# Performance work log

Hardware: AMD Instinct MI355X
Metric: run time of the kernel (lower is better)

## Reference

```python
import jax, jax.numpy as jnp
import numpy as np

B, N, H, D = 16, 128, 32, 5            # graphs, entities, heads, multi_hop_max_dist
NUM_EDGES, NUM_SPATIAL, NUM_EDGE_DIS = 1536, 512, 128
HID, NEF = 768, 3                       # hidden dim (unused in math), edge feats


def setup_inputs() -> dict:
    key = jax.random.key(0)
    ks = jax.random.split(key, 8)
    x = jax.random.normal(ks[0], (B, N, HID), jnp.float32)
    attn_bias = jax.random.normal(ks[1], (B, N + 1, N + 1), jnp.float32)
    spatial_pos = jax.random.randint(ks[2], (B, N, N), 0, NUM_SPATIAL)
    edge_input = jax.random.randint(ks[3], (B, N, N, D, NEF), 0, NUM_EDGES + 1)
    # embedding tables (std=0.02 init; padding_idx=0 rows zeroed)
    edge_encoder_w = (0.02 * jax.random.normal(ks[4], (NUM_EDGES + 1, H), jnp.float32)).at[0].set(0.0)
    structural_w = (0.02 * jax.random.normal(ks[5], (NUM_SPATIAL, H), jnp.float32)).at[0].set(0.0)
    edge_dis_w = 0.02 * jax.random.normal(ks[6], (NUM_EDGE_DIS * H * H, 1), jnp.float32)
    virt_w = 0.02 * jax.random.normal(ks[7], (1, H), jnp.float32)
    return {"x": x, "attn_bias": attn_bias, "spatial_pos": spatial_pos,
            "edge_input": edge_input, "edge_encoder_w": edge_encoder_w,
            "structural_w": structural_w, "edge_dis_w": edge_dis_w, "virt_w": virt_w}


def reference(x, attn_bias, spatial_pos, edge_input, edge_encoder_w, structural_w, edge_dis_w, virt_w):
    n_graph, n_entity = x.shape[:2]
    # [B, H, N+1, N+1]
    bias = jnp.broadcast_to(attn_bias[:, None], (n_graph, H, n_entity + 1, n_entity + 1))
    # structural (spatial) encoding on the NxN sub-block
    sp_bias = structural_w[spatial_pos].transpose(0, 3, 1, 2)          # [B,H,N,N]
    bias = bias.at[:, :, 1:, 1:].add(sp_bias)
    # graph-token virtual distance
    t = virt_w.reshape(1, H, 1)
    bias = bias.at[:, :, 1:, 0].add(t)
    bias = bias.at[:, :, 0, :].add(t)
    # ---- multi_hop relational encoding ----
    sp = jnp.where(spatial_pos == 0, 1, spatial_pos)
    sp = jnp.where(sp > 1, sp - 1, sp)
    sp = jnp.clip(sp, 0, D)                                            # [B,N,N]
    ei = edge_input[:, :, :, :D, :]                                    # [B,N,N,D,F]
    ei = edge_encoder_w[ei].mean(-2)                                   # [B,N,N,D,H]
    # per-hop head-mixing: bmm over hop dim
    Wdis = edge_dis_w.reshape(-1, H, H)[:D]                            # [D,H,H]
    ei = jnp.einsum('bijdh,dhk->bijdk', ei, Wdis)                      # [B,N,N,D,H]
    ei = ei.sum(-2) / sp[..., None].astype(ei.dtype)                   # [B,N,N,H]
    ei = ei.transpose(0, 3, 1, 2)                                      # [B,H,N,N]
    bias = bias.at[:, :, 1:, 1:].add(ei)
    # final residual add of raw attn_bias
    bias = bias + attn_bias[:, None]
    return bias
```

## Files before the change

kernel.cpp:

```cpp
#include <hip/hip_runtime.h>
#include <hip/hip_bf16.h>

#define B_   16
#define N_   128
#define H_   32
#define D_   5
#define NE1  1537
#define NP1  129

#define QSCALE   2.857142857e-3f
#define QINV     350.0f

#define FQ_BYTES   (D_ * NE1 * 16)
#define FQ_DWORDS  (FQ_BYTES / 4)
#define ST_DWORDS  (512 * 32 * 2 / 4)
#define TOT_DWORDS (FQ_DWORDS + ST_DWORDS)
#define TOT_QUADS  (TOT_DWORDS / 4)

static __device__ __forceinline__ float bits2f(unsigned int u) {
    union { unsigned int ui; float f; } cv; cv.ui = u; return cv.f;
}

struct __attribute__((packed, aligned(4))) pk4 { int x, y, z, w; };
struct __attribute__((packed, aligned(4))) pk2 { int x, y; };

__global__ __launch_bounds__(256) void fused_tab_kernel(
    const float* __restrict__ edge_encoder_w,
    const float* __restrict__ edge_dis_w,
    const float* __restrict__ structural_w,
    unsigned char* __restrict__ fused_q,
    unsigned short* __restrict__ st_bf16)
{
    __shared__ float wd[32 * 32];
    const int tid = threadIdx.x;
    const int bx  = blockIdx.x;

    if (bx >= 965) {
        const int e = (bx - 965) * 256 + tid;
        if (e < 512 * 32) {
            st_bf16[e] = (unsigned short)(
                __hip_bfloat16_raw(__float2bfloat16(structural_w[e])).x);
        }
        return;
    }

    const int d     = bx / 193;
    const int chunk = bx % 193;

    const float* wsrc = edge_dis_w + d * 1024;
    for (int k = tid; k < 1024; k += 256) wd[k] = wsrc[k];
    __syncthreads();

    const int g    = tid >> 5;
    const int lane = tid & 31;
    const int idx  = chunk * 8 + g;
    if (idx >= NE1) return;

    float w = edge_encoder_w[idx * 32 + lane];
    float acc = 0.f;
    #pragma unroll
    for (int hh = 0; hh < 32; ++hh) {
        acc += __shfl(w, hh, 32) * wd[hh * 32 + lane];
    }

    int q = (int)__builtin_rintf(acc * QINV);
    q = (q > 7) ? 7 : ((q < -7) ? -7 : q);
    q += 8;

    const int v0 = __shfl(q, 2 * lane,     32);
    const int v1 = __shfl(q, 2 * lane + 1, 32);
    if (lane < 16) {
        fused_q[(d * NE1 + idx) * 16 + lane] = (unsigned char)(v0 | (v1 << 4));
    }
}

__global__ __launch_bounds__(1024) void main_kernel(
    const float* __restrict__ attn_bias,
    const int*   __restrict__ spatial_pos,
    const int*   __restrict__ edge_input,
    const uint4* __restrict__ wsrc,
    float* __restrict__ out)
{
    __shared__ __align__(16) unsigned int lds[TOT_DWORDS];

    const int tid = threadIdx.x;
    const int bx  = blockIdx.x;

    uint4* ldsq = (uint4*)lds;
    for (int k = tid; k < TOT_QUADS; k += 1024) ldsq[k] = wsrc[k];
    __syncthreads();

    const int cell = bx * 1024 + tid;
    const int b = cell >> 14;
    const int i = (cell >> 7) & 127;
    const int j = cell & 127;

    const int* eip = edge_input + cell * 15;
    const pk4 e03  = *(const pk4*)(eip);
    const pk4 e47  = *(const pk4*)(eip + 4);
    const pk4 e8b  = *(const pk4*)(eip + 8);
    const pk2 ecd  = *(const pk2*)(eip + 12);
    const int ee   = eip[14];
    const int eidx[15] = { e03.x, e03.y, e03.z, e03.w,
                           e47.x, e47.y, e47.z, e47.w,
                           e8b.x, e8b.y, e8b.z, e8b.w,
                           ecd.x, ecd.y, ee };

    const int sp0  = spatial_pos[cell];
    const float ab2 = 2.0f * attn_bias[(b * NP1 + (i + 1)) * NP1 + (j + 1)];

    unsigned int aL0 = 0, aL1 = 0, aL2 = 0, aL3 = 0;
    unsigned int aH0 = 0, aH1 = 0, aH2 = 0, aH3 = 0;
    #pragma unroll
    for (int t = 0; t < 15; ++t) {
        const int d  = t / 3;
        const int ro = (d * NE1 + eidx[t]) * 4;
        const uint4 r = *(const uint4*)&lds[ro];
        aL0 += r.x & 0x0F0F0F0Fu;  aH0 += (r.x >> 4) & 0x0F0F0F0Fu;
        aL1 += r.y & 0x0F0F0F0Fu;  aH1 += (r.y >> 4) & 0x0F0F0F0Fu;
        aL2 += r.z & 0x0F0F0F0Fu;  aH2 += (r.z >> 4) & 0x0F0F0F0Fu;
        aL3 += r.w & 0x0F0F0F0Fu;  aH3 += (r.w >> 4) & 0x0F0F0F0Fu;
    }

    int s = sp0; if (s == 0) s = 1; if (s > 1) s -= 1; if (s > D_) s = D_;
    const float kq = QSCALE * __builtin_amdgcn_rcpf(3.0f * (float)s);
    const float C  = ab2 - 120.0f * kq;

    const uint4* stq = (const uint4*)&lds[FQ_DWORDS];
    const uint4 SQ[4] = { stq[sp0 * 4 + 0], stq[sp0 * 4 + 1],
                          stq[sp0 * 4 + 2], stq[sp0 * 4 + 3] };

    const int obase = (b * 32) * (NP1 * NP1) + (i + 1) * NP1 + (j + 1);
    const unsigned int AL[4] = {aL0, aL1, aL2, aL3};
    const unsigned int AH[4] = {aH0, aH1, aH2, aH3};

    #pragma unroll
    for (int q = 0; q < 4; ++q) {
        const unsigned int sdw[4] = {SQ[q].x, SQ[q].y, SQ[q].z, SQ[q].w};
        #pragma unroll
        for (int bb = 0; bb < 4; ++bb) {
            const int hE = 8 * q + 2 * bb;
            const float stE = bits2f(sdw[bb] << 16) + C;
            const float stO = bits2f(sdw[bb] & 0xFFFF0000u) + C;
            const float vE = (float)((AL[q] >> (8 * bb)) & 255u);
            const float vO = (float)((AH[q] >> (8 * bb)) & 255u);
            out[obase + hE * (NP1 * NP1)]       = vE * kq + stE;
            out[obase + (hE + 1) * (NP1 * NP1)] = vO * kq + stO;
        }
    }
}

__global__ __launch_bounds__(256) void border_kernel(
    const float* __restrict__ attn_bias,
    const float* __restrict__ virt_w,
    float* __restrict__ out)
{
    const int bh = blockIdx.x;
    const int b = bh >> 5;
    const int h = bh & 31;
    const float t = virt_w[h];

    float*       ob = out + (b * H_ + h) * NP1 * NP1;
    const float* ab = attn_bias + b * NP1 * NP1;

    for (int idx = threadIdx.x; idx < NP1 + N_; idx += 256) {
        if (idx < NP1) {
            ob[idx] = 2.0f * ab[idx] + t;
        } else {
            const int i = idx - 128;
            ob[i * NP1] = 2.0f * ab[i * NP1] + t;
        }
    }
}

extern "C" void kernel_launch(void* const* d_in, const int* in_sizes, int n_in,
                              void* d_out, int out_size, void* d_ws, size_t ws_size,
                              hipStream_t stream) {
    const float* attn_bias      = (const float*)d_in[1];
    const int*   spatial_pos    = (const int*)  d_in[2];
    const int*   edge_input     = (const int*)  d_in[3];
    const float* edge_encoder_w = (const float*)d_in[4];
    const float* structural_w   = (const float*)d_in[5];
    const float* edge_dis_w     = (const float*)d_in[6];
    const float* virt_w         = (const float*)d_in[7];
    float* out = (float*)d_out;

    unsigned char*  fused_q = (unsigned char*)d_ws;
    unsigned short* st_bf16 = (unsigned short*)((char*)d_ws + FQ_BYTES);

    hipLaunchKernelGGL(fused_tab_kernel, dim3(965 + 64), dim3(256), 0, stream,
                       edge_encoder_w, edge_dis_w, structural_w,
                       fused_q, st_bf16);
    hipLaunchKernelGGL(main_kernel, dim3(256), dim3(1024), 0, stream,
                       attn_bias, spatial_pos, edge_input,
                       (const uint4*)d_ws, out);
    hipLaunchKernelGGL(border_kernel, dim3(B_ * H_), dim3(256), 0, stream,
                       attn_bias, virt_w, out);
}
```

Before: 102.0 us.

## Split head dimension across blocks to halve LDS table and fuse border kernel

Lays out the quantized fused edge table and the bf16 structural table in two head-half regions, so each main-kernel block stages only half the tables in LDS (about 78KB instead of 156KB). The grid doubles to 512 blocks, each handling 16 heads for 1024 cells, which should allow more resident blocks per CU and overlap the prologue table load with the edge_input and attn_bias loads. The border (virtual-token row/column) writes are folded into the main kernel, removing one launch. In exchange, edge_input and spatial_pos are read twice, once per head half, and the table staging is done twice as often across the grid.

```diff
diff --git a/kernel.cpp b/kernel.cpp
--- a/kernel.cpp
+++ b/kernel.cpp
@@ -11,11 +11,13 @@
 #define QSCALE   2.857142857e-3f
 #define QINV     350.0f
 
-#define FQ_BYTES   (D_ * NE1 * 16)
-#define FQ_DWORDS  (FQ_BYTES / 4)
-#define ST_DWORDS  (512 * 32 * 2 / 4)
-#define TOT_DWORDS (FQ_DWORDS + ST_DWORDS)
-#define TOT_QUADS  (TOT_DWORDS / 4)
+#define HT_ROWS    (D_ * NE1)
+#define HT_BYTES   61488
+#define HT_DWORDS  (HT_BYTES / 4)
+#define ST_BYTES   16384
+#define REG_BYTES  (HT_BYTES + ST_BYTES)
+#define REG_DWORDS (REG_BYTES / 4)
+#define REG_QUADS  (REG_DWORDS / 4)
 
 static __device__ __forceinline__ float bits2f(unsigned int u) {
     union { unsigned int ui; float f; } cv; cv.ui = u; return cv.f;
@@ -28,8 +30,7 @@
     const float* __restrict__ edge_encoder_w,
     const float* __restrict__ edge_dis_w,
     const float* __restrict__ structural_w,
-    unsigned char* __restrict__ fused_q,
-    unsigned short* __restrict__ st_bf16)
+    unsigned char* __restrict__ ws)
 {
     __shared__ float wd[32 * 32];
     const int tid = threadIdx.x;
@@ -38,8 +39,12 @@
     if (bx >= 965) {
         const int e = (bx - 965) * 256 + tid;
         if (e < 512 * 32) {
-            st_bf16[e] = (unsigned short)(
+            const int sp = e >> 5, h = e & 31;
+            const int half = h >> 4;
+            unsigned short v = (unsigned short)(
                 __hip_bfloat16_raw(__float2bfloat16(structural_w[e])).x);
+            *(unsigned short*)(ws + half * REG_BYTES + HT_BYTES
+                               + (sp * 16 + (h & 15)) * 2) = v;
         }
         return;
     }
@@ -70,30 +75,32 @@
     const int v0 = __shfl(q, 2 * lane,     32);
     const int v1 = __shfl(q, 2 * lane + 1, 32);
     if (lane < 16) {
-        fused_q[(d * NE1 + idx) * 16 + lane] = (unsigned char)(v0 | (v1 << 4));
+        const int m    = lane;
+        const int half = m >> 3;
+        const int row  = d * NE1 + idx;
+        ws[half * REG_BYTES + row * 8 + (m & 7)] =
+            (unsigned char)(v0 | (v1 << 4));
     }
 }
 
-__global__ __launch_bounds__(1024) void main_kernel(
+__global__ __launch_bounds__(1024, 8) void main_kernel(
     const float* __restrict__ attn_bias,
     const int*   __restrict__ spatial_pos,
     const int*   __restrict__ edge_input,
-    const uint4* __restrict__ wsrc,
+    const uint4* __restrict__ wsq,
+    const float* __restrict__ virt_w,
     float* __restrict__ out)
 {
-    __shared__ __align__(16) unsigned int lds[TOT_DWORDS];
+    __shared__ __align__(16) unsigned int lds[REG_DWORDS];
 
-    const int tid = threadIdx.x;
-    const int bx  = blockIdx.x;
-
-    uint4* ldsq = (uint4*)lds;
-    for (int k = tid; k < TOT_QUADS; k += 1024) ldsq[k] = wsrc[k];
-    __syncthreads();
-
-    const int cell = bx * 1024 + tid;
+    const int tid  = threadIdx.x;
+    const int bx   = blockIdx.x;
+    const int half = bx & 1;
+    const int cell = (bx >> 1) * 1024 + tid;
     const int b = cell >> 14;
     const int i = (cell >> 7) & 127;
     const int j = cell & 127;
+    const int plane = NP1 * NP1;
 
     const int* eip = edge_input + cell * 15;
     const pk4 e03  = *(const pk4*)(eip);
@@ -101,41 +108,54 @@
     const pk4 e8b  = *(const pk4*)(eip + 8);
     const pk2 ecd  = *(const pk2*)(eip + 12);
     const int ee   = eip[14];
+    const int sp0  = spatial_pos[cell];
+    const float ab2 = 2.0f * attn_bias[(b * NP1 + (i + 1)) * NP1 + (j + 1)];
+
+    const int bb_ = bx >> 5, hh_ = bx & 31;
+    const float tvirt = virt_w[hh_];
+    float abrd = 0.f;
+    if (tid < NP1 + N_) {
+        abrd = (tid < NP1) ? attn_bias[bb_ * plane + tid]
+                           : attn_bias[bb_ * plane + (tid - 128) * NP1];
+    }
+
+    const uint4* src = wsq + half * REG_QUADS;
+    uint4* ldsq = (uint4*)lds;
+    #pragma unroll
+    for (int k = 0; k < 5; ++k) {
+        const int o = tid + k * 1024;
+        if (o < REG_QUADS) ldsq[o] = src[o];
+    }
+    __syncthreads();
+
     const int eidx[15] = { e03.x, e03.y, e03.z, e03.w,
                            e47.x, e47.y, e47.z, e47.w,
                            e8b.x, e8b.y, e8b.z, e8b.w,
                            ecd.x, ecd.y, ee };
 
-    const int sp0  = spatial_pos[cell];
-    const float ab2 = 2.0f * attn_bias[(b * NP1 + (i + 1)) * NP1 + (j + 1)];
-
-    unsigned int aL0 = 0, aL1 = 0, aL2 = 0, aL3 = 0;
-    unsigned int aH0 = 0, aH1 = 0, aH2 = 0, aH3 = 0;
+    unsigned int aL0 = 0, aH0 = 0, aL1 = 0, aH1 = 0;
     #pragma unroll
     for (int t = 0; t < 15; ++t) {
         const int d  = t / 3;
-        const int ro = (d * NE1 + eidx[t]) * 4;
-        const uint4 r = *(const uint4*)&lds[ro];
+        const int ro = (d * NE1 + eidx[t]) * 2;
+        const uint2 r = *(const uint2*)&lds[ro];
         aL0 += r.x & 0x0F0F0F0Fu;  aH0 += (r.x >> 4) & 0x0F0F0F0Fu;
         aL1 += r.y & 0x0F0F0F0Fu;  aH1 += (r.y >> 4) & 0x0F0F0F0Fu;
-        aL2 += r.z & 0x0F0F0F0Fu;  aH2 += (r.z >> 4) & 0x0F0F0F0Fu;
-        aL3 += r.w & 0x0F0F0F0Fu;  aH3 += (r.w >> 4) & 0x0F0F0F0Fu;
     }
 
     int s = sp0; if (s == 0) s = 1; if (s > 1) s -= 1; if (s > D_) s = D_;
     const float kq = QSCALE * __builtin_amdgcn_rcpf(3.0f * (float)s);
     const float C  = ab2 - 120.0f * kq;
 
-    const uint4* stq = (const uint4*)&lds[FQ_DWORDS];
-    const uint4 SQ[4] = { stq[sp0 * 4 + 0], stq[sp0 * 4 + 1],
-                          stq[sp0 * 4 + 2], stq[sp0 * 4 + 3] };
+    const uint4* stq = (const uint4*)&lds[HT_DWORDS];
+    const uint4 SQ[2] = { stq[sp0 * 2], stq[sp0 * 2 + 1] };
 
-    const int obase = (b * 32) * (NP1 * NP1) + (i + 1) * NP1 + (j + 1);
-    const unsigned int AL[4] = {aL0, aL1, aL2, aL3};
-    const unsigned int AH[4] = {aH0, aH1, aH2, aH3};
+    const int obase = (b * 32 + half * 16) * plane + (i + 1) * NP1 + (j + 1);
+    const unsigned int AL[2] = {aL0, aL1};
+    const unsigned int AH[2] = {aH0, aH1};
 
     #pragma unroll
-    for (int q = 0; q < 4; ++q) {
+    for (int q = 0; q < 2; ++q) {
         const unsigned int sdw[4] = {SQ[q].x, SQ[q].y, SQ[q].z, SQ[q].w};
         #pragma unroll
         for (int bb = 0; bb < 4; ++bb) {
@@ -144,32 +164,16 @@
             const float stO = bits2f(sdw[bb] & 0xFFFF0000u) + C;
             const float vE = (float)((AL[q] >> (8 * bb)) & 255u);
             const float vO = (float)((AH[q] >> (8 * bb)) & 255u);
-            out[obase + hE * (NP1 * NP1)]       = vE * kq + stE;
-            out[obase + (hE + 1) * (NP1 * NP1)] = vO * kq + stO;
+            out[obase + hE * plane]       = vE * kq + stE;
+            out[obase + (hE + 1) * plane] = vO * kq + stO;
         }
     }
-}
 
-__global__ __launch_bounds__(256) void border_kernel(
-    const float* __restrict__ attn_bias,
-    const float* __restrict__ virt_w,
-    float* __restrict__ out)
-{
-    const int bh = blockIdx.x;
-    const int b = bh >> 5;
-    const int h = bh & 31;
-    const float t = virt_w[h];
-
-    float*       ob = out + (b * H_ + h) * NP1 * NP1;
-    const float* ab = attn_bias + b * NP1 * NP1;
-
-    for (int idx = threadIdx.x; idx < NP1 + N_; idx += 256) {
-        if (idx < NP1) {
-            ob[idx] = 2.0f * ab[idx] + t;
-        } else {
-            const int i = idx - 128;
-            ob[i * NP1] = 2.0f * ab[i * NP1] + t;
-        }
+    if (tid < NP1 + N_) {
+        const float v = 2.0f * abrd + tvirt;
+        float* ob = out + (bb_ * 32 + hh_) * plane;
+        if (tid < NP1) ob[tid] = v;
+        else           ob[(tid - 128) * NP1] = v;
     }
 }
 
@@ -185,15 +189,10 @@
     const float* virt_w         = (const float*)d_in[7];
     float* out = (float*)d_out;
 
-    unsigned char*  fused_q = (unsigned char*)d_ws;
-    unsigned short* st_bf16 = (unsigned short*)((char*)d_ws + FQ_BYTES);
-
     hipLaunchKernelGGL(fused_tab_kernel, dim3(965 + 64), dim3(256), 0, stream,
                        edge_encoder_w, edge_dis_w, structural_w,
-                       fused_q, st_bf16);
-    hipLaunchKernelGGL(main_kernel, dim3(256), dim3(1024), 0, stream,
+                       (unsigned char*)d_ws);
+    hipLaunchKernelGGL(main_kernel, dim3(512), dim3(1024), 0, stream,
                        attn_bias, spatial_pos, edge_input,
-                       (const uint4*)d_ws, out);
-    hipLaunchKernelGGL(border_kernel, dim3(B_ * H_), dim3(256), 0, stream,
-                       attn_bias, virt_w, out);
+                       (const uint4*)d_ws, virt_w, out);
 }
```

After: 99.22 us. 1.03x faster.
